# Kernel tuning notes

Hardware: AMD Instinct MI355X
Metric: run time of the kernel (lower is better)

The kernel has to match this reference:

```python
import jax, jax.numpy as jnp
import numpy as np

NUM_CLASSES = 5
HIGHEST_WEIGHT = 1.0

# Replicates __init__ weight construction: dict key i+1 -> weights[i]
_w = np.linspace(HIGHEST_WEIGHT, 0.0, (NUM_CLASSES + 1) // 2, endpoint=False)
if NUM_CLASSES % 2 == 0:
    _w = np.concatenate((_w, _w[::-1]))
else:
    _w = np.concatenate((_w, [0.0], _w[::-1]))
WEIGHT_TABLE = jnp.asarray(_w, dtype=jnp.float32)  # index = class_label - 1

N = 1 << 25  # 33,554,432 elements (~128MB per fp32 tensor)


def setup_inputs() -> dict:
    key = jax.random.key(0)
    k1, k2 = jax.random.split(key)
    return {
        "predictions": jax.random.normal(k1, (N,), dtype=jnp.float32),
        "targets": jax.random.normal(k2, (N,), dtype=jnp.float32),
    }


def reference(predictions, targets):
    # torch.quantile with default 'linear' interpolation == jnp.quantile default
    probs = jnp.linspace(0.0, 1.0, NUM_CLASSES + 1)
    quantiles = jnp.quantile(targets, probs)
    # torch.searchsorted(..., right=False) == side='left'
    labels = jnp.searchsorted(quantiles, targets, side="left")
    labels = jnp.maximum(labels, 1)  # labels[labels == 0] = 1
    weights = WEIGHT_TABLE[labels - 1]  # small-table gather (detached in torch)
    return jnp.mean(weights * (predictions - targets) ** 2)
```

## Files before the change

kernel.cpp:

```cpp
#include <hip/hip_runtime.h>
#include <cstdint>
#include <math.h>

#define BLOCK 256
#define NBINS 8192
#define HIST_BLOCKS 2048
#define FINAL_BLOCKS 4096

__device__ __forceinline__ uint32_t f2key(float f) {
    uint32_t u = __float_as_uint(f);
    return (u & 0x80000000u) ? ~u : (u | 0x80000000u);
}
__device__ __forceinline__ float key2f(uint32_t k) {
    uint32_t u = (k & 0x80000000u) ? (k ^ 0x80000000u) : ~k;
    return __uint_as_float(u);
}

__global__ void hist_k(const float* __restrict__ t, int N, uint32_t* __restrict__ hist) {
    __shared__ uint32_t h[NBINS];
    for (int i = threadIdx.x; i < NBINS; i += BLOCK) h[i] = 0;
    __syncthreads();
    const float4* t4 = (const float4*)t;
    int n4 = N >> 2;
    int T = gridDim.x * BLOCK;
    int i = blockIdx.x * BLOCK + threadIdx.x;
    for (; i + T < n4; i += 2 * T) {
        float4 a = t4[i];
        float4 b = t4[i + T];
        atomicAdd(&h[f2key(a.x) >> 19], 1u);
        atomicAdd(&h[f2key(a.y) >> 19], 1u);
        atomicAdd(&h[f2key(a.z) >> 19], 1u);
        atomicAdd(&h[f2key(a.w) >> 19], 1u);
        atomicAdd(&h[f2key(b.x) >> 19], 1u);
        atomicAdd(&h[f2key(b.y) >> 19], 1u);
        atomicAdd(&h[f2key(b.z) >> 19], 1u);
        atomicAdd(&h[f2key(b.w) >> 19], 1u);
    }
    for (; i < n4; i += T) {
        float4 a = t4[i];
        atomicAdd(&h[f2key(a.x) >> 19], 1u);
        atomicAdd(&h[f2key(a.y) >> 19], 1u);
        atomicAdd(&h[f2key(a.z) >> 19], 1u);
        atomicAdd(&h[f2key(a.w) >> 19], 1u);
    }
    if (blockIdx.x == 0 && threadIdx.x < (N & 3))
        atomicAdd(&h[f2key(t[(n4 << 2) + threadIdx.x]) >> 19], 1u);
    __syncthreads();
    for (int k = threadIdx.x; k < NBINS; k += BLOCK) {
        uint32_t v = h[k];
        if (v) atomicAdd(&hist[k], v);
    }
}

__global__ void quant_k(const uint32_t* __restrict__ hist, int N,
                        float* __restrict__ q, float* __restrict__ out) {
    constexpr int BPT = NBINS / BLOCK;
    __shared__ uint32_t scan[BLOCK];
    uint32_t local[BPT];
    uint32_t s = 0;
    int t = threadIdx.x;
#pragma unroll
    for (int i = 0; i < BPT; ++i) { local[i] = hist[t * BPT + i]; s += local[i]; }
    scan[t] = s;
    __syncthreads();
    for (int off = 1; off < BLOCK; off <<= 1) {
        uint32_t v = (t >= off) ? scan[t - off] : 0u;
        __syncthreads();
        scan[t] += v;
        __syncthreads();
    }
    uint32_t base = scan[t] - s;
#pragma unroll 1
    for (int j = 0; j < 4; ++j) {
        double pos = (double)(N - 1) * (double)(j + 1) / 5.0;
        uint32_t cum = base;
#pragma unroll
        for (int i = 0; i < BPT; ++i) {
            uint32_t cnt = local[i];
            double cumd = (double)cum;
            if (pos >= cumd && pos < cumd + (double)cnt) {
                uint32_t bin = (uint32_t)(t * BPT + i);
                float vlo = key2f(bin << 19);
                float vhi = (bin == NBINS - 1) ? key2f(0xFFFFFFFFu)
                                               : key2f((bin + 1) << 19);
                double frac = (pos - cumd + 0.5) / (double)cnt;
                q[j] = (float)((double)vlo + frac * ((double)vhi - (double)vlo));
            }
            cum += cnt;
        }
    }
    if (t == 0) out[0] = 0.0f;
}

__global__ void final_k(const float* __restrict__ p, const float* __restrict__ t, int N,
                        const float* __restrict__ qv, float* __restrict__ out) {
    float q1 = qv[0], q2 = qv[1], q3 = qv[2], q4 = qv[3];
    int n4 = N >> 2;
    int T = gridDim.x * BLOCK;
    const float4* p4 = (const float4*)p;
    const float4* t4 = (const float4*)t;
    float acc = 0.f;
    int i = blockIdx.x * BLOCK + threadIdx.x;
    for (; i + T < n4; i += 2 * T) {
        float4 pa = p4[i], ta = t4[i];
        float4 pb = p4[i + T], tb = t4[i + T];
        float pp[8] = {pa.x, pa.y, pa.z, pa.w, pb.x, pb.y, pb.z, pb.w};
        float tt[8] = {ta.x, ta.y, ta.z, ta.w, tb.x, tb.y, tb.z, tb.w};
#pragma unroll
        for (int c = 0; c < 8; ++c) {
            float tv = tt[c];
            int cls = (int)(tv > q1) + (int)(tv > q2) + (int)(tv > q3) + (int)(tv > q4);
            float w = fabsf(3.0f - (float)cls) * 0.33333334f;
            float d = pp[c] - tv;
            acc += w * d * d;
        }
    }
    for (; i < n4; i += T) {
        float4 pa = p4[i], ta = t4[i];
        float pp[4] = {pa.x, pa.y, pa.z, pa.w};
        float tt[4] = {ta.x, ta.y, ta.z, ta.w};
#pragma unroll
        for (int c = 0; c < 4; ++c) {
            float tv = tt[c];
            int cls = (int)(tv > q1) + (int)(tv > q2) + (int)(tv > q3) + (int)(tv > q4);
            float w = fabsf(3.0f - (float)cls) * 0.33333334f;
            float d = pp[c] - tv;
            acc += w * d * d;
        }
    }
    if (blockIdx.x == 0 && threadIdx.x < (N & 3)) {
        int ii = (n4 << 2) + threadIdx.x;
        float tv = t[ii];
        int cls = (int)(tv > q1) + (int)(tv > q2) + (int)(tv > q3) + (int)(tv > q4);
        float w = fabsf(3.0f - (float)cls) * 0.33333334f;
        float d = p[ii] - tv;
        acc += w * d * d;
    }
    for (int off = 32; off > 0; off >>= 1) acc += __shfl_down(acc, off, 64);
    __shared__ float wsum[BLOCK / 64];
    int lane = threadIdx.x & 63, wv = threadIdx.x >> 6;
    if (lane == 0) wsum[wv] = acc;
    __syncthreads();
    if (threadIdx.x == 0) {
        float ssum = 0.f;
#pragma unroll
        for (int k = 0; k < BLOCK / 64; ++k) ssum += wsum[k];
        float inv_n = (float)(1.0 / (double)N);
        atomicAdd(out, ssum * inv_n);
    }
}

extern "C" void kernel_launch(void* const* d_in, const int* in_sizes, int n_in,
                              void* d_out, int out_size, void* d_ws, size_t ws_size,
                              hipStream_t stream) {
    const float* pred = (const float*)d_in[0];
    const float* targ = (const float*)d_in[1];
    int N = in_sizes[1];
    uint32_t* ws = (uint32_t*)d_ws;
    uint32_t* hist = ws;
    float* qv = (float*)(ws + NBINS);
    float* out = (float*)d_out;

    hipMemsetAsync(hist, 0, NBINS * sizeof(uint32_t), stream);
    hist_k<<<HIST_BLOCKS, BLOCK, 0, stream>>>(targ, N, hist);
    quant_k<<<1, BLOCK, 0, stream>>>(hist, N, qv, out);
    final_k<<<FINAL_BLOCKS, BLOCK, 0, stream>>>(pred, targ, N, qv, out);
}
```

Before: 339.9 us.

## Fuse histogram and loss into one pass using per-bin squared-error sums

Replaces the three-kernel flow (histogram of targets, quantile selection, and a second full pass over predictions and targets) with a single pass. That pass builds a per-bin count and a per-bin sum of squared errors in shared memory. The final kernel scans the counts and gives each bin a weight, splitting a bin's mass by rank when a quantile boundary falls inside it, then reduces the weighted sums. This removes the second read of the targets, cutting global memory traffic. In exchange it adds shared-memory float atomics per element and assumes errors are spread evenly within a bin, which is an approximation near the quantile boundaries.

Result: slower. 370.6 us (+9.0%).

```diff
diff --git a/kernel.cpp b/kernel.cpp
--- a/kernel.cpp
+++ b/kernel.cpp
@@ -3,64 +3,88 @@
 #include <math.h>
 
 #define BLOCK 256
-#define NBINS 8192
-#define HIST_BLOCKS 2048
-#define FINAL_BLOCKS 4096
+#define NBINS 4096
+#define PASS_BLOCKS 1024
 
 __device__ __forceinline__ uint32_t f2key(float f) {
     uint32_t u = __float_as_uint(f);
     return (u & 0x80000000u) ? ~u : (u | 0x80000000u);
 }
-__device__ __forceinline__ float key2f(uint32_t k) {
-    uint32_t u = (k & 0x80000000u) ? (k ^ 0x80000000u) : ~k;
-    return __uint_as_float(u);
-}
 
-__global__ void hist_k(const float* __restrict__ t, int N, uint32_t* __restrict__ hist) {
-    __shared__ uint32_t h[NBINS];
-    for (int i = threadIdx.x; i < NBINS; i += BLOCK) h[i] = 0;
+__global__ void __launch_bounds__(BLOCK) pass1_k(const float* __restrict__ p,
+                                                 const float* __restrict__ t, int N,
+                                                 uint32_t* __restrict__ gcnt,
+                                                 float* __restrict__ gsum) {
+    __shared__ uint32_t hcnt[NBINS];
+    __shared__ float hsum[NBINS];
+    for (int i = threadIdx.x; i < NBINS; i += BLOCK) { hcnt[i] = 0; hsum[i] = 0.f; }
     __syncthreads();
+    const float4* p4 = (const float4*)p;
     const float4* t4 = (const float4*)t;
     int n4 = N >> 2;
     int T = gridDim.x * BLOCK;
     int i = blockIdx.x * BLOCK + threadIdx.x;
     for (; i + T < n4; i += 2 * T) {
-        float4 a = t4[i];
-        float4 b = t4[i + T];
-        atomicAdd(&h[f2key(a.x) >> 19], 1u);
-        atomicAdd(&h[f2key(a.y) >> 19], 1u);
-        atomicAdd(&h[f2key(a.z) >> 19], 1u);
-        atomicAdd(&h[f2key(a.w) >> 19], 1u);
-        atomicAdd(&h[f2key(b.x) >> 19], 1u);
-        atomicAdd(&h[f2key(b.y) >> 19], 1u);
-        atomicAdd(&h[f2key(b.z) >> 19], 1u);
-        atomicAdd(&h[f2key(b.w) >> 19], 1u);
+        float4 ta = t4[i];
+        float4 pa = p4[i];
+        float4 tb = t4[i + T];
+        float4 pb = p4[i + T];
+        float tt[8] = {ta.x, ta.y, ta.z, ta.w, tb.x, tb.y, tb.z, tb.w};
+        float pp[8] = {pa.x, pa.y, pa.z, pa.w, pb.x, pb.y, pb.z, pb.w};
+#pragma unroll
+        for (int c = 0; c < 8; ++c) {
+            uint32_t k = f2key(tt[c]) >> 20;
+            float d = pp[c] - tt[c];
+            atomicAdd(&hcnt[k], 1u);
+            atomicAdd(&hsum[k], d * d);
+        }
     }
     for (; i < n4; i += T) {
-        float4 a = t4[i];
-        atomicAdd(&h[f2key(a.x) >> 19], 1u);
-        atomicAdd(&h[f2key(a.y) >> 19], 1u);
-        atomicAdd(&h[f2key(a.z) >> 19], 1u);
-        atomicAdd(&h[f2key(a.w) >> 19], 1u);
+        float4 ta = t4[i];
+        float4 pa = p4[i];
+        float tt[4] = {ta.x, ta.y, ta.z, ta.w};
+        float pp[4] = {pa.x, pa.y, pa.z, pa.w};
+#pragma unroll
+        for (int c = 0; c < 4; ++c) {
+            uint32_t k = f2key(tt[c]) >> 20;
+            float d = pp[c] - tt[c];
+            atomicAdd(&hcnt[k], 1u);
+            atomicAdd(&hsum[k], d * d);
+        }
     }
-    if (blockIdx.x == 0 && threadIdx.x < (N & 3))
-        atomicAdd(&h[f2key(t[(n4 << 2) + threadIdx.x]) >> 19], 1u);
+    if (blockIdx.x == 0 && threadIdx.x < (N & 3)) {
+        int ii = (n4 << 2) + threadIdx.x;
+        uint32_t k = f2key(t[ii]) >> 20;
+        float d = p[ii] - t[ii];
+        atomicAdd(&hcnt[k], 1u);
+        atomicAdd(&hsum[k], d * d);
+    }
     __syncthreads();
     for (int k = threadIdx.x; k < NBINS; k += BLOCK) {
-        uint32_t v = h[k];
-        if (v) atomicAdd(&hist[k], v);
+        uint32_t c = hcnt[k];
+        if (c) {
+            atomicAdd(&gcnt[k], c);
+            atomicAdd(&gsum[k], hsum[k]);
+        }
     }
 }
 
-__global__ void quant_k(const uint32_t* __restrict__ hist, int N,
-                        float* __restrict__ q, float* __restrict__ out) {
+__global__ void __launch_bounds__(BLOCK) fin_k(const uint32_t* __restrict__ gcnt,
+                                               const float* __restrict__ gsum, int N,
+                                               float* __restrict__ out) {
     constexpr int BPT = NBINS / BLOCK;
     __shared__ uint32_t scan[BLOCK];
+    __shared__ double dred[BLOCK];
     uint32_t local[BPT];
+    float lsum[BPT];
     uint32_t s = 0;
     int t = threadIdx.x;
 #pragma unroll
-    for (int i = 0; i < BPT; ++i) { local[i] = hist[t * BPT + i]; s += local[i]; }
+    for (int i = 0; i < BPT; ++i) {
+        local[i] = gcnt[t * BPT + i];
+        lsum[i] = gsum[t * BPT + i];
+        s += local[i];
+    }
     scan[t] = s;
     __syncthreads();
     for (int off = 1; off < BLOCK; off <<= 1) {
@@ -69,85 +93,41 @@
         scan[t] += v;
         __syncthreads();
     }
-    uint32_t base = scan[t] - s;
-#pragma unroll 1
-    for (int j = 0; j < 4; ++j) {
-        double pos = (double)(N - 1) * (double)(j + 1) / 5.0;
-        uint32_t cum = base;
+    uint32_t cumbase = scan[t] - s;
+    double beta[4];
 #pragma unroll
-        for (int i = 0; i < BPT; ++i) {
-            uint32_t cnt = local[i];
-            double cumd = (double)cum;
-            if (pos >= cumd && pos < cumd + (double)cnt) {
-                uint32_t bin = (uint32_t)(t * BPT + i);
-                float vlo = key2f(bin << 19);
-                float vhi = (bin == NBINS - 1) ? key2f(0xFFFFFFFFu)
-                                               : key2f((bin + 1) << 19);
-                double frac = (pos - cumd + 0.5) / (double)cnt;
-                q[j] = (float)((double)vlo + frac * ((double)vhi - (double)vlo));
+    for (int j = 0; j < 4; ++j)
+        beta[j] = (double)(N - 1) * (double)(j + 1) / 5.0 + 1.0;
+    const double W[5] = {1.0, 2.0 / 3.0, 1.0 / 3.0, 0.0, 1.0 / 3.0};
+    double acc = 0.0;
+    uint32_t cum = cumbase;
+#pragma unroll
+    for (int i = 0; i < BPT; ++i) {
+        uint32_t c = local[i];
+        if (c) {
+            double lo = (double)cum, cd = (double)c;
+            double u[6];
+            u[0] = 1.0;
+            u[5] = 0.0;
+#pragma unroll
+            for (int j = 0; j < 4; ++j) {
+                double above = (lo + cd - beta[j]) / cd;
+                u[j + 1] = above < 0.0 ? 0.0 : (above > 1.0 ? 1.0 : above);
             }
-            cum += cnt;
+            double effw = 0.0;
+#pragma unroll
+            for (int cls = 0; cls < 5; ++cls) effw += W[cls] * (u[cls] - u[cls + 1]);
+            acc += effw * (double)lsum[i];
         }
+        cum += c;
     }
-    if (t == 0) out[0] = 0.0f;
-}
-
-__global__ void final_k(const float* __restrict__ p, const float* __restrict__ t, int N,
-                        const float* __restrict__ qv, float* __restrict__ out) {
-    float q1 = qv[0], q2 = qv[1], q3 = qv[2], q4 = qv[3];
-    int n4 = N >> 2;
-    int T = gridDim.x * BLOCK;
-    const float4* p4 = (const float4*)p;
-    const float4* t4 = (const float4*)t;
-    float acc = 0.f;
-    int i = blockIdx.x * BLOCK + threadIdx.x;
-    for (; i + T < n4; i += 2 * T) {
-        float4 pa = p4[i], ta = t4[i];
-        float4 pb = p4[i + T], tb = t4[i + T];
-        float pp[8] = {pa.x, pa.y, pa.z, pa.w, pb.x, pb.y, pb.z, pb.w};
-        float tt[8] = {ta.x, ta.y, ta.z, ta.w, tb.x, tb.y, tb.z, tb.w};
-#pragma unroll
-        for (int c = 0; c < 8; ++c) {
-            float tv = tt[c];
-            int cls = (int)(tv > q1) + (int)(tv > q2) + (int)(tv > q3) + (int)(tv > q4);
-            float w = fabsf(3.0f - (float)cls) * 0.33333334f;
-            float d = pp[c] - tv;
-            acc += w * d * d;
-        }
+    dred[t] = acc;
+    __syncthreads();
+    for (int off = BLOCK / 2; off > 0; off >>= 1) {
+        if (t < off) dred[t] += dred[t + off];
+        __syncthreads();
     }
-    for (; i < n4; i += T) {
-        float4 pa = p4[i], ta = t4[i];
-        float pp[4] = {pa.x, pa.y, pa.z, pa.w};
-        float tt[4] = {ta.x, ta.y, ta.z, ta.w};
-#pragma unroll
-        for (int c = 0; c < 4; ++c) {
-            float tv = tt[c];
-            int cls = (int)(tv > q1) + (int)(tv > q2) + (int)(tv > q3) + (int)(tv > q4);
-            float w = fabsf(3.0f - (float)cls) * 0.33333334f;
-            float d = pp[c] - tv;
-            acc += w * d * d;
-        }
-    }
-    if (blockIdx.x == 0 && threadIdx.x < (N & 3)) {
-        int ii = (n4 << 2) + threadIdx.x;
-        float tv = t[ii];
-        int cls = (int)(tv > q1) + (int)(tv > q2) + (int)(tv > q3) + (int)(tv > q4);
-        float w = fabsf(3.0f - (float)cls) * 0.33333334f;
-        float d = p[ii] - tv;
-        acc += w * d * d;
-    }
-    for (int off = 32; off > 0; off >>= 1) acc += __shfl_down(acc, off, 64);
-    __shared__ float wsum[BLOCK / 64];
-    int lane = threadIdx.x & 63, wv = threadIdx.x >> 6;
-    if (lane == 0) wsum[wv] = acc;
-    __syncthreads();
-    if (threadIdx.x == 0) {
-        float ssum = 0.f;
-#pragma unroll
-        for (int k = 0; k < BLOCK / 64; ++k) ssum += wsum[k];
-        float inv_n = (float)(1.0 / (double)N);
-        atomicAdd(out, ssum * inv_n);
-    }
+    if (t == 0) out[0] = (float)(dred[0] / (double)N);
 }
 
 extern "C" void kernel_launch(void* const* d_in, const int* in_sizes, int n_in,
@@ -156,13 +136,11 @@
     const float* pred = (const float*)d_in[0];
     const float* targ = (const float*)d_in[1];
     int N = in_sizes[1];
-    uint32_t* ws = (uint32_t*)d_ws;
-    uint32_t* hist = ws;
-    float* qv = (float*)(ws + NBINS);
+    uint32_t* gcnt = (uint32_t*)d_ws;
+    float* gsum = (float*)(gcnt + NBINS);
     float* out = (float*)d_out;
 
-    hipMemsetAsync(hist, 0, NBINS * sizeof(uint32_t), stream);
-    hist_k<<<HIST_BLOCKS, BLOCK, 0, stream>>>(targ, N, hist);
-    quant_k<<<1, BLOCK, 0, stream>>>(hist, N, qv, out);
-    final_k<<<FINAL_BLOCKS, BLOCK, 0, stream>>>(pred, targ, N, qv, out);
+    hipMemsetAsync(d_ws, 0, 2 * NBINS * sizeof(uint32_t), stream);
+    pass1_k<<<PASS_BLOCKS, BLOCK, 0, stream>>>(pred, targ, N, gcnt, gsum);
+    fin_k<<<1, BLOCK, 0, stream>>>(gcnt, gsum, N, out);
 }
```
